# Kernel optimization log

Measured on AMD Instinct MI355X. Metric: run time of the kernel, lower is better.

The kernel has to match this reference:

```python
import jax, jax.numpy as jnp
import numpy as np

B, N, K, C, COUT = 8, 4096, 16, 128, 256
EDGE_IN = 2 * C + 64 + 64  # center | diff | ppf_enc | pos_enc = 384
BN_EPS = 1e-5


def _bn(x, g, b, m, v):
    # eval-mode BatchNorm over channel (last) axis
    return (x - m) * (g / jnp.sqrt(v + BN_EPS)) + b


def setup_inputs() -> dict:
    key = jax.random.key(0)
    ks = jax.random.split(key, 40)
    rn = lambda i, s, sc=1.0: jax.random.normal(ks[i], s, jnp.float32) * sc
    un = lambda i, s: jax.random.uniform(ks[i], s, jnp.float32, 0.5, 1.5)
    inp = {
        "kpt_feature": rn(0, (B, N, C)),
        "kpt_xyz": rn(1, (B, N, 3)),
        "neighbor_feature": rn(2, (B, N, K, C)),
        "neighbor_xyz": rn(3, (B, N, K, 3)),
        "neighbor_normals": rn(4, (B, N, K, 3)),
        # ppf_encoder: Linear(4,32) + BN(32) + ReLU + Linear(32,64)
        "ppf_w1": rn(5, (32, 4), 0.3), "ppf_b1": rn(6, (32,), 0.1),
        "ppf_g": rn(7, (32,), 0.1) + 1.0, "ppf_beta": rn(8, (32,), 0.1),
        "ppf_m": rn(9, (32,), 0.1), "ppf_v": un(10, (32,)),
        "ppf_w2": rn(11, (64, 32), 0.1), "ppf_b2": rn(12, (64,), 0.1),
        # pos_encoder: Conv2d(3,64,1) + BN(64) + ReLU  (1x1 conv == linear)
        "pos_w": rn(13, (64, 3), 0.3), "pos_b": rn(14, (64,), 0.1),
        "pos_g": rn(15, (64,), 0.1) + 1.0, "pos_beta": rn(16, (64,), 0.1),
        "pos_m": rn(17, (64,), 0.1), "pos_v": un(18, (64,)),
        # edge_mlp: Conv2d(384,256,1)+BN+ReLU, Conv2d(256,COUT,1)+BN+ReLU
        "e1_w": rn(19, (256, EDGE_IN), 0.05), "e1_b": rn(20, (256,), 0.1),
        "e1_g": rn(21, (256,), 0.1) + 1.0, "e1_beta": rn(22, (256,), 0.1),
        "e1_m": rn(23, (256,), 0.1), "e1_v": un(24, (256,)),
        "e2_w": rn(25, (COUT, 256), 0.05), "e2_b": rn(26, (COUT,), 0.1),
        "e2_g": rn(27, (COUT,), 0.1) + 1.0, "e2_beta": rn(28, (COUT,), 0.1),
        "e2_m": rn(29, (COUT,), 0.1), "e2_v": un(30, (COUT,)),
    }
    return inp


def reference(kpt_feature, kpt_xyz, neighbor_feature, neighbor_xyz, neighbor_normals,
              ppf_w1, ppf_b1, ppf_g, ppf_beta, ppf_m, ppf_v, ppf_w2, ppf_b2,
              pos_w, pos_b, pos_g, pos_beta, pos_m, pos_v,
              e1_w, e1_b, e1_g, e1_beta, e1_m, e1_v,
              e2_w, e2_b, e2_g, e2_beta, e2_m, e2_v):
    # all tensors kept channels-last: [B, N, K, C]
    center = kpt_feature[:, :, None, :]                       # [B,N,1,C]
    diff = neighbor_feature - center                          # [B,N,K,C]
    rel = neighbor_xyz - kpt_xyz[:, :, None, :]               # [B,N,K,3]

    # pos_encoder (1x1 conv == per-point linear)
    pos_enc = jax.nn.relu(_bn(rel @ pos_w.T + pos_b, pos_g, pos_beta, pos_m, pos_v))  # [B,N,K,64]

    # keypoint normals = normalized mean of neighbor normals
    kn = neighbor_normals.mean(axis=2)
    kn = kn / jnp.maximum(jnp.linalg.norm(kn, axis=-1, keepdims=True), 1e-12)
    n1 = kn[:, :, None, :]                                    # [B,N,1,3]

    # PPF features: [d_norm, n1.d, n2.d, n1.n2]
    d_norm = jnp.linalg.norm(rel, axis=-1, keepdims=True)
    d = rel / (d_norm + 1e-8)
    alpha = jnp.clip(jnp.sum(n1 * d, -1, keepdims=True), -1.0, 1.0)
    phi = jnp.clip(jnp.sum(neighbor_normals * d, -1, keepdims=True), -1.0, 1.0)
    theta = jnp.clip(jnp.sum(n1 * neighbor_normals, -1, keepdims=True), -1.0, 1.0)
    ppf = jnp.concatenate([d_norm, alpha, phi, theta], -1)    # [B,N,K,4]

    h = jax.nn.relu(_bn(ppf @ ppf_w1.T + ppf_b1, ppf_g, ppf_beta, ppf_m, ppf_v))
    ppf_enc = h @ ppf_w2.T + ppf_b2                           # [B,N,K,64]

    edge = jnp.concatenate(
        [jnp.broadcast_to(center, diff.shape), diff, ppf_enc, pos_enc], axis=-1)  # [B,N,K,384]

    h = jax.nn.relu(_bn(edge @ e1_w.T + e1_b, e1_g, e1_beta, e1_m, e1_v))  # [B,N,K,256]
    h = jax.nn.relu(_bn(h @ e2_w.T + e2_b, e2_g, e2_beta, e2_m, e2_v))      # [B,N,K,COUT]
    return h.max(axis=2)                                      # [B,N,COUT]
```

## Files before the change

### kernel.cpp

```cpp
#include <hip/hip_runtime.h>

#define NB 8
#define NN 4096
#define KK 16
#define CC 128
#define NCOUT 256
#define E_IN 384
#define EK 352
#define KS1 22
#define KS2 16
#define EPS 1e-5f

#define WB1_ELEMS (KS1 * 8 * 64 * 8)
#define WB2_ELEMS (KS2 * 8 * 64 * 8)
#define WB2_OFF   (WB1_ELEMS * 2)
#define SMALL_OFF (WB1_ELEMS * 2 + WB2_ELEMS * 2)
#define S_POSW 0
#define S_POSB 192
#define S_W1F 256
#define S_B1F 384
#define S_E1B 416
#define S_E2B 672
#define SMALL_FLOATS 928

typedef __attribute__((ext_vector_type(8))) short bf16x8;
typedef __attribute__((ext_vector_type(16))) float f32x16;

static __device__ __forceinline__ unsigned short f2bf(float f) {
    unsigned u = __float_as_uint(f);
    u += 0x7fffu + ((u >> 16) & 1u);
    return (unsigned short)(u >> 16);
}

__global__ void ppf_prep(
    const float* __restrict__ ppf_w1, const float* __restrict__ ppf_b1,
    const float* __restrict__ ppf_g,  const float* __restrict__ ppf_beta,
    const float* __restrict__ ppf_m,  const float* __restrict__ ppf_v,
    const float* __restrict__ ppf_w2, const float* __restrict__ ppf_b2,
    const float* __restrict__ pos_w,  const float* __restrict__ pos_b,
    const float* __restrict__ pos_g,  const float* __restrict__ pos_beta,
    const float* __restrict__ pos_m,  const float* __restrict__ pos_v,
    const float* __restrict__ e1_w,   const float* __restrict__ e1_b,
    const float* __restrict__ e1_g,   const float* __restrict__ e1_beta,
    const float* __restrict__ e1_m,   const float* __restrict__ e1_v,
    const float* __restrict__ e2_w,   const float* __restrict__ e2_b,
    const float* __restrict__ e2_g,   const float* __restrict__ e2_beta,
    const float* __restrict__ e2_m,   const float* __restrict__ e2_v,
    void* __restrict__ ws)
{
    int idx = blockIdx.x * 256 + threadIdx.x;
    unsigned short* wb1 = (unsigned short*)ws;
    unsigned short* wb2 = (unsigned short*)((char*)ws + WB2_OFF);
    float* sm = (float*)((char*)ws + SMALL_OFF);

    if (idx < WB1_ELEMS) {
        int t = idx >> 12;
        int c = (idx >> 9) & 7;
        int l = (idx >> 3) & 63;
        int j = idx & 7;
        int o = c * 32 + (l & 31);
        int i = t * 16 + ((l >> 5) << 3) + j;
        float s = e1_g[o] * rsqrtf(e1_v[o] + EPS);
        float v;
        if (i < 256) {
            v = e1_w[o * E_IN + i];
        } else if (i < 288) {
            int jj = i - 256;
            float a = 0.f;
            for (int p = 0; p < 64; ++p)
                a += e1_w[o * E_IN + 256 + p] * ppf_w2[p * 32 + jj];
            v = a;
        } else {
            v = e1_w[o * E_IN + (i + 32)];
        }
        wb1[idx] = f2bf(v * s);
    } else if (idx < WB1_ELEMS + WB2_ELEMS) {
        int e = idx - WB1_ELEMS;
        int t = e >> 12;
        int c = (e >> 9) & 7;
        int l = (e >> 3) & 63;
        int j = e & 7;
        int o = c * 32 + (l & 31);
        int i = t * 16 + ((l >> 5) << 3) + j;
        float s = e2_g[o] * rsqrtf(e2_v[o] + EPS);
        wb2[e] = f2bf(e2_w[o * NCOUT + i] * s);
    } else if (idx < WB1_ELEMS + WB2_ELEMS + SMALL_FLOATS) {
        int s = idx - (WB1_ELEMS + WB2_ELEMS);
        float v;
        if (s < 192) {
            int o = s / 3, c2 = s - o * 3;
            float sc = pos_g[o] * rsqrtf(pos_v[o] + EPS);
            v = pos_w[o * 3 + c2] * sc;
        } else if (s < 256) {
            int o = s - 192;
            float sc = pos_g[o] * rsqrtf(pos_v[o] + EPS);
            v = (pos_b[o] - pos_m[o]) * sc + pos_beta[o];
        } else if (s < 384) {
            int q = s - 256; int j = q >> 2, i = q & 3;
            float sc = ppf_g[j] * rsqrtf(ppf_v[j] + EPS);
            v = ppf_w1[j * 4 + i] * sc;
        } else if (s < 416) {
            int j = s - 384;
            float sc = ppf_g[j] * rsqrtf(ppf_v[j] + EPS);
            v = (ppf_b1[j] - ppf_m[j]) * sc + ppf_beta[j];
        } else if (s < 672) {
            int o = s - 416;
            float sc = e1_g[o] * rsqrtf(e1_v[o] + EPS);
            float bb = e1_b[o];
            for (int p = 0; p < 64; ++p)
                bb += e1_w[o * E_IN + 256 + p] * ppf_b2[p];
            v = (bb - e1_m[o]) * sc + e1_beta[o];
        } else {
            int o = s - 672;
            float sc = e2_g[o] * rsqrtf(e2_v[o] + EPS);
            v = (e2_b[o] - e2_m[o]) * sc + e2_beta[o];
        }
        sm[s] = v;
    }
}

__global__ __launch_bounds__(256, 3) void ppf_main(
    const float* __restrict__ kptf, const float* __restrict__ kptx,
    const float* __restrict__ nbrf, const float* __restrict__ nbrx,
    const float* __restrict__ nbrn, const void* __restrict__ ws,
    float* __restrict__ out)
{
    __shared__ __align__(16) char smem[64 * EK * 2];
    __shared__ float rel_lds[64][4];
    __shared__ float smallw[SMALL_FLOATS];

    const int tid = threadIdx.x;
    const int lane = tid & 63;
    const int w = tid >> 6;
    const int l31 = lane & 31;
    const int h5 = lane >> 5;
    const long g0 = (long)blockIdx.x * 4;

    const unsigned short* wB1 = (const unsigned short*)ws;
    const unsigned short* wB2 = (const unsigned short*)((const char*)ws + WB2_OFF);
    const float* smallg = (const float*)((const char*)ws + SMALL_OFF);

    for (int i = tid; i < SMALL_FLOATS; i += 256) smallw[i] = smallg[i];

    #pragma unroll
    for (int it = 0; it < 4; ++it) {
        int chunk = tid + it * 256;
        int r = chunk >> 4, cj = chunk & 15;
        int gl = r >> 4, k = r & 15;
        long g = g0 + gl;
        const float4* cp = (const float4*)(kptf + g * CC + cj * 8);
        const float4* np = (const float4*)(nbrf + (g * KK + k) * CC + cj * 8);
        float4 c0 = cp[0], c1 = cp[1];
        float4 n0 = np[0], n1 = np[1];
        float cfv[8] = {c0.x, c0.y, c0.z, c0.w, c1.x, c1.y, c1.z, c1.w};
        float nfv[8] = {n0.x, n0.y, n0.z, n0.w, n1.x, n1.y, n1.z, n1.w};
        bf16x8 vc, vd;
        #pragma unroll
        for (int j = 0; j < 8; ++j) {
            vc[j] = (short)f2bf(cfv[j]);
            vd[j] = (short)f2bf(nfv[j] - cfv[j]);
        }
        int swz = (r & 7) << 4;
        *(bf16x8*)(smem + ((r * (EK * 2) + cj * 16) ^ swz)) = vc;
        *(bf16x8*)(smem + ((r * (EK * 2) + 256 + cj * 16) ^ swz)) = vd;
    }
    __syncthreads();

    if (w == 0) {
        int r = lane, gl = r >> 4, k = r & 15;
        long g = g0 + gl;
        const float* nxp = nbrx + (g * KK + k) * 3;
        const float* kxp = kptx + g * 3;
        const float* nnp = nbrn + (g * KK + k) * 3;
        float rx = nxp[0] - kxp[0], ry = nxp[1] - kxp[1], rz = nxp[2] - kxp[2];
        float ax = nnp[0], ay = nnp[1], az = nnp[2];
        rel_lds[r][0] = rx; rel_lds[r][1] = ry; rel_lds[r][2] = rz;
        float sx = ax, sy = ay, sz = az;
        #pragma unroll
        for (int m = 1; m < 16; m <<= 1) {
            sx += __shfl_xor(sx, m);
            sy += __shfl_xor(sy, m);
            sz += __shfl_xor(sz, m);
        }
        sx *= 0.0625f; sy *= 0.0625f; sz *= 0.0625f;
        float kl = fmaxf(sqrtf(sx * sx + sy * sy + sz * sz), 1e-12f);
        float inv = 1.0f / kl;
        float knx = sx * inv, kny = sy * inv, knz = sz * inv;
        float dn = sqrtf(rx * rx + ry * ry + rz * rz);
        float di = 1.0f / (dn + 1e-8f);
        float dx = rx * di, dy = ry * di, dz = rz * di;
        float alpha = fminf(fmaxf(knx * dx + kny * dy + knz * dz, -1.f), 1.f);
        float phi   = fminf(fmaxf(ax * dx + ay * dy + az * dz, -1.f), 1.f);
        float theta = fminf(fmaxf(knx * ax + kny * ay + knz * az, -1.f), 1.f);
        int swz = (r & 7) << 4;
        #pragma unroll
        for (int q = 0; q < 4; ++q) {
            bf16x8 hv;
            #pragma unroll
            for (int u = 0; u < 8; ++u) {
                int j = q * 8 + u;
                const float* wr = &smallw[S_W1F + j * 4];
                float v = dn * wr[0] + alpha * wr[1] + phi * wr[2] + theta * wr[3]
                          + smallw[S_B1F + j];
                hv[u] = (short)f2bf(fmaxf(v, 0.f));
            }
            *(bf16x8*)(smem + ((r * (EK * 2) + 512 + q * 16) ^ swz)) = hv;
        }
    }
    __syncthreads();

    {
        int col = tid & 63;
        int rbase = tid >> 6;
        float w0 = smallw[S_POSW + col * 3];
        float w1 = smallw[S_POSW + col * 3 + 1];
        float w2v = smallw[S_POSW + col * 3 + 2];
        float pb = smallw[S_POSB + col];
        #pragma unroll
        for (int i = 0; i < 16; ++i) {
            int r = rbase + i * 4;
            float v = fmaxf(rel_lds[r][0] * w0 + rel_lds[r][1] * w1 + rel_lds[r][2] * w2v + pb, 0.f);
            *(unsigned short*)(smem + ((r * (EK * 2) + 576 + col * 2) ^ ((r & 7) << 4))) = f2bf(v);
        }
    }
    __syncthreads();

    f32x16 acc[2][2];
    #pragma unroll
    for (int a = 0; a < 2; ++a)
        #pragma unroll
        for (int b = 0; b < 2; ++b)
            #pragma unroll
            for (int q = 0; q < 16; ++q) acc[a][b][q] = 0.f;

    {
        const int kofs = h5 << 4;
        for (int t = 0; t < KS1; ++t) {
            int r0 = l31, r1 = 32 + l31;
            bf16x8 a0 = *(const bf16x8*)(smem + ((r0 * (EK * 2) + t * 32 + kofs) ^ ((r0 & 7) << 4)));
            bf16x8 a1 = *(const bf16x8*)(smem + ((r1 * (EK * 2) + t * 32 + kofs) ^ ((r1 & 7) << 4)));
            const unsigned short* wp = wB1 + (size_t)((t * 8 + 2 * w) * 64 + lane) * 8;
            bf16x8 b0 = *(const bf16x8*)wp;
            bf16x8 b1 = *(const bf16x8*)(wp + 512);
            acc[0][0] = __builtin_amdgcn_mfma_f32_32x32x16_bf16(a0, b0, acc[0][0], 0, 0, 0);
            acc[0][1] = __builtin_amdgcn_mfma_f32_32x32x16_bf16(a0, b1, acc[0][1], 0, 0, 0);
            acc[1][0] = __builtin_amdgcn_mfma_f32_32x32x16_bf16(a1, b0, acc[1][0], 0, 0, 0);
            acc[1][1] = __builtin_amdgcn_mfma_f32_32x32x16_bf16(a1, b1, acc[1][1], 0, 0, 0);
        }
    }
    __syncthreads();

    #pragma unroll
    for (int rf = 0; rf < 2; ++rf)
        #pragma unroll
        for (int cf = 0; cf < 2; ++cf) {
            int c = (2 * w + cf) * 32 + l31;
            float bias = smallw[S_E1B + c];
            #pragma unroll
            for (int reg = 0; reg < 16; ++reg) {
                int row = rf * 32 + (reg & 3) + ((reg >> 2) << 3) + (h5 << 2);
                float v = fmaxf(acc[rf][cf][reg] + bias, 0.f);
                *(unsigned short*)(smem + ((row * 512 + c * 2) ^ ((row & 7) << 4))) = f2bf(v);
            }
        }
    __syncthreads();

    #pragma unroll
    for (int a = 0; a < 2; ++a)
        #pragma unroll
        for (int b = 0; b < 2; ++b)
            #pragma unroll
            for (int q = 0; q < 16; ++q) acc[a][b][q] = 0.f;
    {
        const int kofs = h5 << 4;
        for (int t = 0; t < KS2; ++t) {
            int r0 = l31, r1 = 32 + l31;
            bf16x8 a0 = *(const bf16x8*)(smem + ((r0 * 512 + t * 32 + kofs) ^ ((r0 & 7) << 4)));
            bf16x8 a1 = *(const bf16x8*)(smem + ((r1 * 512 + t * 32 + kofs) ^ ((r1 & 7) << 4)));
            const unsigned short* wp = wB2 + (size_t)((t * 8 + 2 * w) * 64 + lane) * 8;
            bf16x8 b0 = *(const bf16x8*)wp;
            bf16x8 b1 = *(const bf16x8*)(wp + 512);
            acc[0][0] = __builtin_amdgcn_mfma_f32_32x32x16_bf16(a0, b0, acc[0][0], 0, 0, 0);
            acc[0][1] = __builtin_amdgcn_mfma_f32_32x32x16_bf16(a0, b1, acc[0][1], 0, 0, 0);
            acc[1][0] = __builtin_amdgcn_mfma_f32_32x32x16_bf16(a1, b0, acc[1][0], 0, 0, 0);
            acc[1][1] = __builtin_amdgcn_mfma_f32_32x32x16_bf16(a1, b1, acc[1][1], 0, 0, 0);
        }
    }

    #pragma unroll
    for (int rf = 0; rf < 2; ++rf)
        #pragma unroll
        for (int cf = 0; cf < 2; ++cf) {
            int c = (2 * w + cf) * 32 + l31;
            float bias = smallw[S_E2B + c];
            #pragma unroll
            for (int gs = 0; gs < 2; ++gs) {
                float m = acc[rf][cf][gs * 8];
                #pragma unroll
                for (int q = 1; q < 8; ++q) m = fmaxf(m, acc[rf][cf][gs * 8 + q]);
                m = fmaxf(m + bias, 0.f);
                m = fmaxf(m, __shfl_xor(m, 32));
                if (lane < 32) {
                    long g = g0 + rf * 2 + gs;
                    out[g * NCOUT + c] = m;
                }
            }
        }
}

extern "C" void kernel_launch(void* const* d_in, const int* in_sizes, int n_in,
                              void* d_out, int out_size, void* d_ws, size_t ws_size,
                              hipStream_t stream)
{
    const float* kptf = (const float*)d_in[0];
    const float* kptx = (const float*)d_in[1];
    const float* nbrf = (const float*)d_in[2];
    const float* nbrx = (const float*)d_in[3];
    const float* nbrn = (const float*)d_in[4];

    int prep_total = WB1_ELEMS + WB2_ELEMS + SMALL_FLOATS;
    ppf_prep<<<dim3((prep_total + 255) / 256), dim3(256), 0, stream>>>(
        (const float*)d_in[5],  (const float*)d_in[6],  (const float*)d_in[7],
        (const float*)d_in[8],  (const float*)d_in[9],  (const float*)d_in[10],
        (const float*)d_in[11], (const float*)d_in[12], (const float*)d_in[13],
        (const float*)d_in[14], (const float*)d_in[15], (const float*)d_in[16],
        (const float*)d_in[17], (const float*)d_in[18], (const float*)d_in[19],
        (const float*)d_in[20], (const float*)d_in[21], (const float*)d_in[22],
        (const float*)d_in[23], (const float*)d_in[24], (const float*)d_in[25],
        (const float*)d_in[26], (const float*)d_in[27], (const float*)d_in[28],
        (const float*)d_in[29], (const float*)d_in[30], d_ws);

    ppf_main<<<dim3((NB * NN) / 4), dim3(256), 0, stream>>>(
        kptf, kptx, nbrf, nbrx, nbrn, d_ws, (float*)d_out);
}
```

Before: 545.9 us.

## Factor center-feature GEMM into per-point pass and shrink edge GEMM K

Uses the identity center·Wc + (nbr−center)·Wd = center·(Wc−Wd) + nbr·Wd to compute the center term once per keypoint in a new cc_gemm kernel, which writes it plus the layer-1 bias into the output buffer. The main kernel reads that term back as its accumulator init and runs layer 1 over only 224 inputs (14 K-steps) instead of 352 (22). This removes the per-neighbor center loads, the diff computation and part of the MFMA work, at the cost of an extra launch and a round trip through global memory. The GEMM loops also gain register double-buffering of A/B fragments, and the small-weight LDS staging is replaced by direct global reads.

```diff
diff --git a/kernel.cpp b/kernel.cpp
--- a/kernel.cpp
+++ b/kernel.cpp
@@ -6,21 +6,23 @@
 #define CC 128
 #define NCOUT 256
 #define E_IN 384
-#define EK 352
-#define KS1 22
+#define KS1 14
 #define KS2 16
+#define KSC 8
 #define EPS 1e-5f
 
 #define WB1_ELEMS (KS1 * 8 * 64 * 8)
 #define WB2_ELEMS (KS2 * 8 * 64 * 8)
+#define WCC_ELEMS (KSC * 8 * 64 * 8)
 #define WB2_OFF   (WB1_ELEMS * 2)
-#define SMALL_OFF (WB1_ELEMS * 2 + WB2_ELEMS * 2)
+#define WCC_OFF   (WB2_OFF + WB2_ELEMS * 2)
+#define SMALL_OFF (WCC_OFF + WCC_ELEMS * 2)
 #define S_POSW 0
 #define S_POSB 192
 #define S_W1F 256
 #define S_B1F 384
-#define S_E1B 416
-#define S_E2B 672
+#define S_E2B 416
+#define S_E1B 672
 #define SMALL_FLOATS 928
 
 typedef __attribute__((ext_vector_type(8))) short bf16x8;
@@ -51,136 +53,208 @@
     int idx = blockIdx.x * 256 + threadIdx.x;
     unsigned short* wb1 = (unsigned short*)ws;
     unsigned short* wb2 = (unsigned short*)((char*)ws + WB2_OFF);
+    unsigned short* wcc = (unsigned short*)((char*)ws + WCC_OFF);
     float* sm = (float*)((char*)ws + SMALL_OFF);
 
     if (idx < WB1_ELEMS) {
-        int t = idx >> 12;
-        int c = (idx >> 9) & 7;
-        int l = (idx >> 3) & 63;
-        int j = idx & 7;
+        int t = idx >> 12, c = (idx >> 9) & 7, l = (idx >> 3) & 63, j = idx & 7;
         int o = c * 32 + (l & 31);
         int i = t * 16 + ((l >> 5) << 3) + j;
         float s = e1_g[o] * rsqrtf(e1_v[o] + EPS);
         float v;
-        if (i < 256) {
-            v = e1_w[o * E_IN + i];
-        } else if (i < 288) {
-            int jj = i - 256;
+        if (i < 128) {
+            v = e1_w[o * E_IN + 128 + i];
+        } else if (i < 160) {
+            int q = i - 128;
             float a = 0.f;
             for (int p = 0; p < 64; ++p)
-                a += e1_w[o * E_IN + 256 + p] * ppf_w2[p * 32 + jj];
+                a += e1_w[o * E_IN + 256 + p] * ppf_w2[p * 32 + q];
             v = a;
         } else {
-            v = e1_w[o * E_IN + (i + 32)];
+            v = e1_w[o * E_IN + 160 + i];
         }
         wb1[idx] = f2bf(v * s);
     } else if (idx < WB1_ELEMS + WB2_ELEMS) {
         int e = idx - WB1_ELEMS;
-        int t = e >> 12;
-        int c = (e >> 9) & 7;
-        int l = (e >> 3) & 63;
-        int j = e & 7;
+        int t = e >> 12, c = (e >> 9) & 7, l = (e >> 3) & 63, j = e & 7;
         int o = c * 32 + (l & 31);
         int i = t * 16 + ((l >> 5) << 3) + j;
         float s = e2_g[o] * rsqrtf(e2_v[o] + EPS);
         wb2[e] = f2bf(e2_w[o * NCOUT + i] * s);
-    } else if (idx < WB1_ELEMS + WB2_ELEMS + SMALL_FLOATS) {
-        int s = idx - (WB1_ELEMS + WB2_ELEMS);
+    } else if (idx < WB1_ELEMS + WB2_ELEMS + WCC_ELEMS) {
+        int e = idx - (WB1_ELEMS + WB2_ELEMS);
+        int t = e >> 12, c = (e >> 9) & 7, l = (e >> 3) & 63, j = e & 7;
+        int o = c * 32 + (l & 31);
+        int i = t * 16 + ((l >> 5) << 3) + j;
+        float s = e1_g[o] * rsqrtf(e1_v[o] + EPS);
+        wcc[e] = f2bf((e1_w[o * E_IN + i] - e1_w[o * E_IN + 128 + i]) * s);
+    } else if (idx < WB1_ELEMS + WB2_ELEMS + WCC_ELEMS + SMALL_FLOATS) {
+        int s = idx - (WB1_ELEMS + WB2_ELEMS + WCC_ELEMS);
         float v;
         if (s < 192) {
             int o = s / 3, c2 = s - o * 3;
-            float sc = pos_g[o] * rsqrtf(pos_v[o] + EPS);
-            v = pos_w[o * 3 + c2] * sc;
+            v = pos_w[o * 3 + c2] * (pos_g[o] * rsqrtf(pos_v[o] + EPS));
         } else if (s < 256) {
             int o = s - 192;
             float sc = pos_g[o] * rsqrtf(pos_v[o] + EPS);
             v = (pos_b[o] - pos_m[o]) * sc + pos_beta[o];
         } else if (s < 384) {
             int q = s - 256; int j = q >> 2, i = q & 3;
-            float sc = ppf_g[j] * rsqrtf(ppf_v[j] + EPS);
-            v = ppf_w1[j * 4 + i] * sc;
+            v = ppf_w1[j * 4 + i] * (ppf_g[j] * rsqrtf(ppf_v[j] + EPS));
         } else if (s < 416) {
             int j = s - 384;
             float sc = ppf_g[j] * rsqrtf(ppf_v[j] + EPS);
             v = (ppf_b1[j] - ppf_m[j]) * sc + ppf_beta[j];
         } else if (s < 672) {
             int o = s - 416;
+            float sc = e2_g[o] * rsqrtf(e2_v[o] + EPS);
+            v = (e2_b[o] - e2_m[o]) * sc + e2_beta[o];
+        } else {
+            int o = s - 672;
             float sc = e1_g[o] * rsqrtf(e1_v[o] + EPS);
             float bb = e1_b[o];
             for (int p = 0; p < 64; ++p)
                 bb += e1_w[o * E_IN + 256 + p] * ppf_b2[p];
             v = (bb - e1_m[o]) * sc + e1_beta[o];
-        } else {
-            int o = s - 672;
-            float sc = e2_g[o] * rsqrtf(e2_v[o] + EPS);
-            v = (e2_b[o] - e2_m[o]) * sc + e2_beta[o];
         }
         sm[s] = v;
     }
 }
 
-__global__ __launch_bounds__(256, 3) void ppf_main(
-    const float* __restrict__ kptf, const float* __restrict__ kptx,
-    const float* __restrict__ nbrf, const float* __restrict__ nbrx,
-    const float* __restrict__ nbrn, const void* __restrict__ ws,
-    float* __restrict__ out)
+__global__ __launch_bounds__(256, 3) void cc_gemm(
+    const float* __restrict__ kptf, const void* __restrict__ ws, float* __restrict__ out)
 {
-    __shared__ __align__(16) char smem[64 * EK * 2];
-    __shared__ float rel_lds[64][4];
-    __shared__ float smallw[SMALL_FLOATS];
-
+    __shared__ __align__(16) char smem[64 * 256];
     const int tid = threadIdx.x;
     const int lane = tid & 63;
     const int w = tid >> 6;
-    const int l31 = lane & 31;
-    const int h5 = lane >> 5;
+    const int l31 = lane & 31, h5 = lane >> 5;
+    const long p0 = (long)blockIdx.x * 64;
+    const unsigned short* wCC = (const unsigned short*)((const char*)ws + WCC_OFF);
+    const float* smallg = (const float*)((const char*)ws + SMALL_OFF);
+
+    {
+        int r = tid >> 2, q = tid & 3;
+        const float4* kp = (const float4*)(kptf + (p0 + r) * CC + q * 32);
+        float4 kf[8];
+        #pragma unroll
+        for (int u = 0; u < 8; ++u) kf[u] = kp[u];
+        int base = r * 256, swz = (r & 7) << 4;
+        #pragma unroll
+        for (int u2 = 0; u2 < 4; ++u2) {
+            bf16x8 v;
+            const float4 f0 = kf[2 * u2], f1 = kf[2 * u2 + 1];
+            v[0] = (short)f2bf(f0.x); v[1] = (short)f2bf(f0.y);
+            v[2] = (short)f2bf(f0.z); v[3] = (short)f2bf(f0.w);
+            v[4] = (short)f2bf(f1.x); v[5] = (short)f2bf(f1.y);
+            v[6] = (short)f2bf(f1.z); v[7] = (short)f2bf(f1.w);
+            *(bf16x8*)(smem + ((base + q * 64 + u2 * 16) ^ swz)) = v;
+        }
+    }
+    float bias0 = smallg[S_E1B + (2 * w + 0) * 32 + l31];
+    float bias1 = smallg[S_E1B + (2 * w + 1) * 32 + l31];
+    __syncthreads();
+
+    f32x16 acc[2][2];
+    #pragma unroll
+    for (int rf = 0; rf < 2; ++rf) {
+        #pragma unroll
+        for (int q = 0; q < 16; ++q) { acc[rf][0][q] = bias0; acc[rf][1][q] = bias1; }
+    }
+
+    const int a0base = l31 * 256 + h5 * 16;
+    const int a1base = (32 + l31) * 256 + h5 * 16;
+    const int aswz = (l31 & 7) << 4;
+    const unsigned short* wp = wCC + (size_t)(2 * w * 64 + lane) * 8;
+
+    bf16x8 a0 = *(const bf16x8*)(smem + (a0base ^ aswz));
+    bf16x8 a1 = *(const bf16x8*)(smem + (a1base ^ aswz));
+    bf16x8 b0 = *(const bf16x8*)wp;
+    bf16x8 b1 = *(const bf16x8*)(wp + 512);
+    #pragma unroll 2
+    for (int t = 0; t < KSC - 1; ++t) {
+        bf16x8 a0n = *(const bf16x8*)(smem + ((a0base + (t + 1) * 32) ^ aswz));
+        bf16x8 a1n = *(const bf16x8*)(smem + ((a1base + (t + 1) * 32) ^ aswz));
+        const unsigned short* wpn = wp + (size_t)(t + 1) * 4096;
+        bf16x8 b0n = *(const bf16x8*)wpn;
+        bf16x8 b1n = *(const bf16x8*)(wpn + 512);
+        acc[0][0] = __builtin_amdgcn_mfma_f32_32x32x16_bf16(a0, b0, acc[0][0], 0, 0, 0);
+        acc[0][1] = __builtin_amdgcn_mfma_f32_32x32x16_bf16(a0, b1, acc[0][1], 0, 0, 0);
+        acc[1][0] = __builtin_amdgcn_mfma_f32_32x32x16_bf16(a1, b0, acc[1][0], 0, 0, 0);
+        acc[1][1] = __builtin_amdgcn_mfma_f32_32x32x16_bf16(a1, b1, acc[1][1], 0, 0, 0);
+        a0 = a0n; a1 = a1n; b0 = b0n; b1 = b1n;
+    }
+    acc[0][0] = __builtin_amdgcn_mfma_f32_32x32x16_bf16(a0, b0, acc[0][0], 0, 0, 0);
+    acc[0][1] = __builtin_amdgcn_mfma_f32_32x32x16_bf16(a0, b1, acc[0][1], 0, 0, 0);
+    acc[1][0] = __builtin_amdgcn_mfma_f32_32x32x16_bf16(a1, b0, acc[1][0], 0, 0, 0);
+    acc[1][1] = __builtin_amdgcn_mfma_f32_32x32x16_bf16(a1, b1, acc[1][1], 0, 0, 0);
+
+    #pragma unroll
+    for (int rf = 0; rf < 2; ++rf)
+        #pragma unroll
+        for (int cf = 0; cf < 2; ++cf) {
+            int c = (2 * w + cf) * 32 + l31;
+            #pragma unroll
+            for (int reg = 0; reg < 16; ++reg) {
+                int row = rf * 32 + (reg & 3) + ((reg >> 2) << 3) + (h5 << 2);
+                out[(p0 + row) * NCOUT + c] = acc[rf][cf][reg];
+            }
+        }
+}
+
+__global__ __launch_bounds__(256, 3) void ppf_main(
+    const float* __restrict__ kptx, const float* __restrict__ nbrf,
+    const float* __restrict__ nbrx, const float* __restrict__ nbrn,
+    const void* __restrict__ ws, float* out)
+{
+    __shared__ __align__(16) char smem[64 * 512];
+    __shared__ float rel_lds[64][4];
+
+    const int tid = threadIdx.x;
+    const int lane = tid & 63;
+    const int w = tid >> 6;
+    const int l31 = lane & 31, h5 = lane >> 5;
     const long g0 = (long)blockIdx.x * 4;
 
     const unsigned short* wB1 = (const unsigned short*)ws;
     const unsigned short* wB2 = (const unsigned short*)((const char*)ws + WB2_OFF);
     const float* smallg = (const float*)((const char*)ws + SMALL_OFF);
 
-    for (int i = tid; i < SMALL_FLOATS; i += 256) smallw[i] = smallg[i];
-
-    #pragma unroll
-    for (int it = 0; it < 4; ++it) {
-        int chunk = tid + it * 256;
-        int r = chunk >> 4, cj = chunk & 15;
-        int gl = r >> 4, k = r & 15;
-        long g = g0 + gl;
-        const float4* cp = (const float4*)(kptf + g * CC + cj * 8);
-        const float4* np = (const float4*)(nbrf + (g * KK + k) * CC + cj * 8);
-        float4 c0 = cp[0], c1 = cp[1];
-        float4 n0 = np[0], n1 = np[1];
-        float cfv[8] = {c0.x, c0.y, c0.z, c0.w, c1.x, c1.y, c1.z, c1.w};
-        float nfv[8] = {n0.x, n0.y, n0.z, n0.w, n1.x, n1.y, n1.z, n1.w};
-        bf16x8 vc, vd;
-        #pragma unroll
-        for (int j = 0; j < 8; ++j) {
-            vc[j] = (short)f2bf(cfv[j]);
-            vd[j] = (short)f2bf(nfv[j] - cfv[j]);
-        }
-        int swz = (r & 7) << 4;
-        *(bf16x8*)(smem + ((r * (EK * 2) + cj * 16) ^ swz)) = vc;
-        *(bf16x8*)(smem + ((r * (EK * 2) + 256 + cj * 16) ^ swz)) = vd;
-    }
-    __syncthreads();
-
-    if (w == 0) {
-        int r = lane, gl = r >> 4, k = r & 15;
-        long g = g0 + gl;
+    const int cr = tid >> 2, cq = tid & 3;
+    const long cg = g0 + (cr >> 4);
+    const float4* nfp = (const float4*)(nbrf + (cg * KK + (cr & 15)) * CC + cq * 32);
+    float4 nf[8];
+    #pragma unroll
+    for (int u = 0; u < 8; ++u) nf[u] = nfp[u];
+
+    float ccv[2][2][2];
+    #pragma unroll
+    for (int rf = 0; rf < 2; ++rf)
+        #pragma unroll
+        for (int cf = 0; cf < 2; ++cf)
+            #pragma unroll
+            for (int hf = 0; hf < 2; ++hf)
+                ccv[rf][cf][hf] = out[(g0 + 2 * rf + hf) * NCOUT + (2 * w + cf) * 32 + l31];
+
+    float pw0 = smallg[S_POSW + lane * 3];
+    float pw1 = smallg[S_POSW + lane * 3 + 1];
+    float pw2 = smallg[S_POSW + lane * 3 + 2];
+    float pb  = smallg[S_POSB + lane];
+
+    {
+        const long g = g0 + w;
+        const int k = lane & 15;
+        const int r = w * 16 + k;
         const float* nxp = nbrx + (g * KK + k) * 3;
-        const float* kxp = kptx + g * 3;
         const float* nnp = nbrn + (g * KK + k) * 3;
-        float rx = nxp[0] - kxp[0], ry = nxp[1] - kxp[1], rz = nxp[2] - kxp[2];
+        float kx0 = kptx[g * 3], kx1 = kptx[g * 3 + 1], kx2 = kptx[g * 3 + 2];
+        float rx = nxp[0] - kx0, ry = nxp[1] - kx1, rz = nxp[2] - kx2;
         float ax = nnp[0], ay = nnp[1], az = nnp[2];
         rel_lds[r][0] = rx; rel_lds[r][1] = ry; rel_lds[r][2] = rz;
         float sx = ax, sy = ay, sz = az;
         #pragma unroll
         for (int m = 1; m < 16; m <<= 1) {
-            sx += __shfl_xor(sx, m);
-            sy += __shfl_xor(sy, m);
-            sz += __shfl_xor(sz, m);
+            sx += __shfl_xor(sx, m); sy += __shfl_xor(sy, m); sz += __shfl_xor(sz, m);
         }
         sx *= 0.0625f; sy *= 0.0625f; sz *= 0.0625f;
         float kl = fmaxf(sqrtf(sx * sx + sy * sy + sz * sz), 1e-12f);
@@ -192,61 +266,84 @@
         float alpha = fminf(fmaxf(knx * dx + kny * dy + knz * dz, -1.f), 1.f);
         float phi   = fminf(fmaxf(ax * dx + ay * dy + az * dz, -1.f), 1.f);
         float theta = fminf(fmaxf(knx * ax + kny * ay + knz * az, -1.f), 1.f);
-        int swz = (r & 7) << 4;
+        int base = r * 448, swz = (r & 7) << 4;
         #pragma unroll
         for (int q = 0; q < 4; ++q) {
             bf16x8 hv;
             #pragma unroll
             for (int u = 0; u < 8; ++u) {
                 int j = q * 8 + u;
-                const float* wr = &smallw[S_W1F + j * 4];
-                float v = dn * wr[0] + alpha * wr[1] + phi * wr[2] + theta * wr[3]
-                          + smallw[S_B1F + j];
+                float v = dn    * smallg[S_W1F + j * 4]
+                        + alpha * smallg[S_W1F + j * 4 + 1]
+                        + phi   * smallg[S_W1F + j * 4 + 2]
+                        + theta * smallg[S_W1F + j * 4 + 3]
+                        + smallg[S_B1F + j];
                 hv[u] = (short)f2bf(fmaxf(v, 0.f));
             }
-            *(bf16x8*)(smem + ((r * (EK * 2) + 512 + q * 16) ^ swz)) = hv;
+            *(bf16x8*)(smem + ((base + 256 + q * 16) ^ swz)) = hv;
+        }
+    }
+
+    {
+        int base = cr * 448, swz = (cr & 7) << 4;
+        #pragma unroll
+        for (int u2 = 0; u2 < 4; ++u2) {
+            bf16x8 v;
+            const float4 f0 = nf[2 * u2], f1 = nf[2 * u2 + 1];
+            v[0] = (short)f2bf(f0.x); v[1] = (short)f2bf(f0.y);
+            v[2] = (short)f2bf(f0.z); v[3] = (short)f2bf(f0.w);
+            v[4] = (short)f2bf(f1.x); v[5] = (short)f2bf(f1.y);
+            v[6] = (short)f2bf(f1.z); v[7] = (short)f2bf(f1.w);
+            *(bf16x8*)(smem + ((base + cq * 64 + u2 * 16) ^ swz)) = v;
         }
     }
     __syncthreads();
 
     {
-        int col = tid & 63;
-        int rbase = tid >> 6;
-        float w0 = smallw[S_POSW + col * 3];
-        float w1 = smallw[S_POSW + col * 3 + 1];
-        float w2v = smallw[S_POSW + col * 3 + 2];
-        float pb = smallw[S_POSB + col];
         #pragma unroll
         for (int i = 0; i < 16; ++i) {
-            int r = rbase + i * 4;
-            float v = fmaxf(rel_lds[r][0] * w0 + rel_lds[r][1] * w1 + rel_lds[r][2] * w2v + pb, 0.f);
-            *(unsigned short*)(smem + ((r * (EK * 2) + 576 + col * 2) ^ ((r & 7) << 4))) = f2bf(v);
+            int r = w + i * 4;
+            float v = fmaxf(rel_lds[r][0] * pw0 + rel_lds[r][1] * pw1 + rel_lds[r][2] * pw2 + pb, 0.f);
+            *(unsigned short*)(smem + ((r * 448 + 320 + lane * 2) ^ ((r & 7) << 4))) = f2bf(v);
         }
     }
     __syncthreads();
 
     f32x16 acc[2][2];
     #pragma unroll
-    for (int a = 0; a < 2; ++a)
-        #pragma unroll
-        for (int b = 0; b < 2; ++b)
-            #pragma unroll
-            for (int q = 0; q < 16; ++q) acc[a][b][q] = 0.f;
-
-    {
-        const int kofs = h5 << 4;
-        for (int t = 0; t < KS1; ++t) {
-            int r0 = l31, r1 = 32 + l31;
-            bf16x8 a0 = *(const bf16x8*)(smem + ((r0 * (EK * 2) + t * 32 + kofs) ^ ((r0 & 7) << 4)));
-            bf16x8 a1 = *(const bf16x8*)(smem + ((r1 * (EK * 2) + t * 32 + kofs) ^ ((r1 & 7) << 4)));
-            const unsigned short* wp = wB1 + (size_t)((t * 8 + 2 * w) * 64 + lane) * 8;
-            bf16x8 b0 = *(const bf16x8*)wp;
-            bf16x8 b1 = *(const bf16x8*)(wp + 512);
+    for (int rf = 0; rf < 2; ++rf)
+        #pragma unroll
+        for (int cf = 0; cf < 2; ++cf)
+            #pragma unroll
+            for (int q = 0; q < 16; ++q)
+                acc[rf][cf][q] = ccv[rf][cf][q >> 3];
+
+    {
+        const int a0base = l31 * 448 + h5 * 16;
+        const int a1base = (32 + l31) * 448 + h5 * 16;
+        const int aswz = (l31 & 7) << 4;
+        const unsigned short* wp = wB1 + (size_t)(2 * w * 64 + lane) * 8;
+        bf16x8 a0 = *(const bf16x8*)(smem + (a0base ^ aswz));
+        bf16x8 a1 = *(const bf16x8*)(smem + (a1base ^ aswz));
+        bf16x8 b0 = *(const bf16x8*)wp;
+        bf16x8 b1 = *(const bf16x8*)(wp + 512);
+        #pragma unroll 2
+        for (int t = 0; t < KS1 - 1; ++t) {
+            bf16x8 a0n = *(const bf16x8*)(smem + ((a0base + (t + 1) * 32) ^ aswz));
+            bf16x8 a1n = *(const bf16x8*)(smem + ((a1base + (t + 1) * 32) ^ aswz));
+            const unsigned short* wpn = wp + (size_t)(t + 1) * 4096;
+            bf16x8 b0n = *(const bf16x8*)wpn;
+            bf16x8 b1n = *(const bf16x8*)(wpn + 512);
             acc[0][0] = __builtin_amdgcn_mfma_f32_32x32x16_bf16(a0, b0, acc[0][0], 0, 0, 0);
             acc[0][1] = __builtin_amdgcn_mfma_f32_32x32x16_bf16(a0, b1, acc[0][1], 0, 0, 0);
             acc[1][0] = __builtin_amdgcn_mfma_f32_32x32x16_bf16(a1, b0, acc[1][0], 0, 0, 0);
             acc[1][1] = __builtin_amdgcn_mfma_f32_32x32x16_bf16(a1, b1, acc[1][1], 0, 0, 0);
-        }
+            a0 = a0n; a1 = a1n; b0 = b0n; b1 = b1n;
+        }
+        acc[0][0] = __builtin_amdgcn_mfma_f32_32x32x16_bf16(a0, b0, acc[0][0], 0, 0, 0);
+        acc[0][1] = __builtin_amdgcn_mfma_f32_32x32x16_bf16(a0, b1, acc[0][1], 0, 0, 0);
+        acc[1][0] = __builtin_amdgcn_mfma_f32_32x32x16_bf16(a1, b0, acc[1][0], 0, 0, 0);
+        acc[1][1] = __builtin_amdgcn_mfma_f32_32x32x16_bf16(a1, b1, acc[1][1], 0, 0, 0);
     }
     __syncthreads();
 
@@ -255,36 +352,48 @@
         #pragma unroll
         for (int cf = 0; cf < 2; ++cf) {
             int c = (2 * w + cf) * 32 + l31;
-            float bias = smallw[S_E1B + c];
             #pragma unroll
             for (int reg = 0; reg < 16; ++reg) {
                 int row = rf * 32 + (reg & 3) + ((reg >> 2) << 3) + (h5 << 2);
-                float v = fmaxf(acc[rf][cf][reg] + bias, 0.f);
-                *(unsigned short*)(smem + ((row * 512 + c * 2) ^ ((row & 7) << 4))) = f2bf(v);
+                *(unsigned short*)(smem + ((row * 512 + c * 2) ^ ((row & 7) << 4))) =
+                    f2bf(fmaxf(acc[rf][cf][reg], 0.f));
             }
         }
     __syncthreads();
 
     #pragma unroll
-    for (int a = 0; a < 2; ++a)
-        #pragma unroll
-        for (int b = 0; b < 2; ++b)
-            #pragma unroll
-            for (int q = 0; q < 16; ++q) acc[a][b][q] = 0.f;
-    {
-        const int kofs = h5 << 4;
-        for (int t = 0; t < KS2; ++t) {
-            int r0 = l31, r1 = 32 + l31;
-            bf16x8 a0 = *(const bf16x8*)(smem + ((r0 * 512 + t * 32 + kofs) ^ ((r0 & 7) << 4)));
-            bf16x8 a1 = *(const bf16x8*)(smem + ((r1 * 512 + t * 32 + kofs) ^ ((r1 & 7) << 4)));
-            const unsigned short* wp = wB2 + (size_t)((t * 8 + 2 * w) * 64 + lane) * 8;
-            bf16x8 b0 = *(const bf16x8*)wp;
-            bf16x8 b1 = *(const bf16x8*)(wp + 512);
+    for (int rf = 0; rf < 2; ++rf)
+        #pragma unroll
+        for (int cf = 0; cf < 2; ++cf)
+            #pragma unroll
+            for (int q = 0; q < 16; ++q)
+                acc[rf][cf][q] = 0.f;
+    {
+        const int a0base = l31 * 512 + h5 * 16;
+        const int a1base = (32 + l31) * 512 + h5 * 16;
+        const int aswz = (l31 & 7) << 4;
+        const unsigned short* wp = wB2 + (size_t)(2 * w * 64 + lane) * 8;
+        bf16x8 a0 = *(const bf16x8*)(smem + (a0base ^ aswz));
+        bf16x8 a1 = *(const bf16x8*)(smem + (a1base ^ aswz));
+        bf16x8 b0 = *(const bf16x8*)wp;
+        bf16x8 b1 = *(const bf16x8*)(wp + 512);
+        #pragma unroll 2
+        for (int t = 0; t < KS2 - 1; ++t) {
+            bf16x8 a0n = *(const bf16x8*)(smem + ((a0base + (t + 1) * 32) ^ aswz));
+            bf16x8 a1n = *(const bf16x8*)(smem + ((a1base + (t + 1) * 32) ^ aswz));
+            const unsigned short* wpn = wp + (size_t)(t + 1) * 4096;
+            bf16x8 b0n = *(const bf16x8*)wpn;
+            bf16x8 b1n = *(const bf16x8*)(wpn + 512);
             acc[0][0] = __builtin_amdgcn_mfma_f32_32x32x16_bf16(a0, b0, acc[0][0], 0, 0, 0);
             acc[0][1] = __builtin_amdgcn_mfma_f32_32x32x16_bf16(a0, b1, acc[0][1], 0, 0, 0);
             acc[1][0] = __builtin_amdgcn_mfma_f32_32x32x16_bf16(a1, b0, acc[1][0], 0, 0, 0);
             acc[1][1] = __builtin_amdgcn_mfma_f32_32x32x16_bf16(a1, b1, acc[1][1], 0, 0, 0);
-        }
+            a0 = a0n; a1 = a1n; b0 = b0n; b1 = b1n;
+        }
+        acc[0][0] = __builtin_amdgcn_mfma_f32_32x32x16_bf16(a0, b0, acc[0][0], 0, 0, 0);
+        acc[0][1] = __builtin_amdgcn_mfma_f32_32x32x16_bf16(a0, b1, acc[0][1], 0, 0, 0);
+        acc[1][0] = __builtin_amdgcn_mfma_f32_32x32x16_bf16(a1, b0, acc[1][0], 0, 0, 0);
+        acc[1][1] = __builtin_amdgcn_mfma_f32_32x32x16_bf16(a1, b1, acc[1][1], 0, 0, 0);
     }
 
     #pragma unroll
@@ -292,7 +401,7 @@
         #pragma unroll
         for (int cf = 0; cf < 2; ++cf) {
             int c = (2 * w + cf) * 32 + l31;
-            float bias = smallw[S_E2B + c];
+            float bias = smallg[S_E2B + c];
             #pragma unroll
             for (int gs = 0; gs < 2; ++gs) {
                 float m = acc[rf][cf][gs * 8];
@@ -318,7 +427,7 @@
     const float* nbrx = (const float*)d_in[3];
     const float* nbrn = (const float*)d_in[4];
 
-    int prep_total = WB1_ELEMS + WB2_ELEMS + SMALL_FLOATS;
+    int prep_total = WB1_ELEMS + WB2_ELEMS + WCC_ELEMS + SMALL_FLOATS;
     ppf_prep<<<dim3((prep_total + 255) / 256), dim3(256), 0, stream>>>(
         (const float*)d_in[5],  (const float*)d_in[6],  (const float*)d_in[7],
         (const float*)d_in[8],  (const float*)d_in[9],  (const float*)d_in[10],
@@ -330,6 +439,8 @@
         (const float*)d_in[26], (const float*)d_in[27], (const float*)d_in[28],
         (const float*)d_in[29], (const float*)d_in[30], d_ws);
 
+    cc_gemm<<<dim3((NB * NN) / 64), dim3(256), 0, stream>>>(kptf, d_ws, (float*)d_out);
+
     ppf_main<<<dim3((NB * NN) / 4), dim3(256), 0, stream>>>(
-        kptf, kptx, nbrf, nbrx, nbrn, d_ws, (float*)d_out);
+        kptx, nbrf, nbrx, nbrn, d_ws, (float*)d_out);
 }
```

After: 530.7 us. 1.03x faster.
